# Kernel tuning notes

Measured on AMD Instinct MI355X. Metric: run time of the kernel, lower is better.

Reference implementation:

```python
import jax, jax.numpy as jnp
import numpy as np

NUM_ITERS = 5
NUM_SPATIAL = 3          # S: xyz spatial dims
THETA_ALPHA = 1.0
THETA_BETA = 1.0
THETA_GAMMA = 8.0


def _gauss_filter(f, q):
    """Exact Gaussian filtering (math the permutohedral lattice pl.apply approximates).
    f: [D, N] features, q: [C, N] values.
    out[:, i] = sum_j exp(-0.5 * ||f_i - f_j||^2) * q[:, j]
    """
    f2 = jnp.sum(f * f, axis=0)                       # [N]
    d2 = f2[:, None] + f2[None, :] - 2.0 * (f.T @ f)  # [N, N] squared distances
    K = jnp.exp(-0.5 * d2)                            # symmetric Gaussian kernel
    return q @ K                                      # [C, N]


def setup_inputs() -> dict:
    key = jax.random.key(0)
    k1, k2 = jax.random.split(key)
    C, N, D = 10, 8192, 6
    unaries = jax.random.normal(k1, (C, N), dtype=jnp.float32)
    feat = jax.random.normal(k2, (D, N), dtype=jnp.float32)
    # learned params: diagonal init for filter weights, Potts (-I) compatibility
    spatial_weights = jnp.eye(C, dtype=jnp.float32)
    bilateral_weights = jnp.eye(C, dtype=jnp.float32)
    compatibility_matrix = -jnp.eye(C, dtype=jnp.float32)
    return {
        "unaries": unaries,
        "feat": feat,
        "spatial_weights": spatial_weights,
        "bilateral_weights": bilateral_weights,
        "compatibility_matrix": compatibility_matrix,
    }


def reference(unaries, feat, spatial_weights, bilateral_weights, compatibility_matrix):
    # Pre-scaled features (torch code scales per-iteration, but with
    # theta_alpha=theta_beta=1.0 the in-place aliasing division is a no-op).
    sp_feat = feat[:NUM_SPATIAL] / THETA_GAMMA                      # [S, N]
    bl_feat = jnp.concatenate(
        [feat[:NUM_SPATIAL] / THETA_ALPHA, feat[NUM_SPATIAL:] / THETA_BETA],
        axis=0,
    )                                                               # [S+F, N]

    q = unaries
    for _ in range(NUM_ITERS):
        p = jax.nn.softmax(q, axis=0)                               # over classes
        spatial_out = _gauss_filter(sp_feat, p)                     # [C, N]
        bilateral_out = _gauss_filter(bl_feat, p)                   # [C, N]
        message_passing = spatial_weights @ spatial_out + bilateral_weights @ bilateral_out
        pairwise = compatibility_matrix @ message_passing
        q = unaries - pairwise
    return q
```

## Files before the change

### kernel.cpp

```cpp
#include <hip/hip_runtime.h>
#include <math.h>

#define N 8192
#define C 10
#define NUM_ITERS 5
#define FBLOCK 1024
#define IBLK 32
#define NBLK (N / IBLK)
#define JW (N / 16)
#define NS (JW / 32)
#define LOG2E 1.44269504088896340736f
#define C3 (LOG2E / 64.0f)

typedef _Float16 half8 __attribute__((ext_vector_type(8)));
typedef _Float16 half4 __attribute__((ext_vector_type(4)));
typedef _Float16 half2 __attribute__((ext_vector_type(2)));
typedef float f32x4 __attribute__((ext_vector_type(4)));
typedef float f32x16 __attribute__((ext_vector_type(16)));

#define WS_AJS 0
#define WS_AJB (N * 16)
#define WS_PF0 (N * 32)
#define WS_PF1 (N * 64)
#define PFIDX(n, c) ((((n) >> 4) * 16 + (c)) * 16 + ((n) & 15))

static __device__ __forceinline__ unsigned int pkexp(float a, float b) {
    float ea = __builtin_amdgcn_exp2f(a);
    float eb = __builtin_amdgcn_exp2f(b);
    return __builtin_bit_cast(unsigned int, __builtin_amdgcn_cvt_pkrtz(ea, eb));
}

static __device__ __forceinline__ half8 rdfrag(const unsigned int* R, int q) {
    uint2 lo = *(const uint2*)&R[2 * q];
    uint2 hi = *(const uint2*)&R[8 + 2 * q];
    half2 a = __builtin_bit_cast(half2, lo.x);
    half2 b = __builtin_bit_cast(half2, lo.y);
    half2 c = __builtin_bit_cast(half2, hi.x);
    half2 d = __builtin_bit_cast(half2, hi.y);
    half8 r = {a[0], a[1], b[0], b[1], c[0], c[1], d[0], d[1]};
    return r;
}

__global__ __launch_bounds__(256) void init_kernel(
    const float* __restrict__ unaries, const float* __restrict__ feat,
    half8* __restrict__ ajs8, half8* __restrict__ ajb8,
    _Float16* __restrict__ pf0, _Float16* __restrict__ pf1) {
    int n = blockIdx.x * 256 + threadIdx.x;
    float f6[6];
#pragma unroll
    for (int d = 0; d < 6; ++d) f6[d] = feat[d * N + n];
    float h3 = 0.5f * (f6[0] * f6[0] + f6[1] * f6[1] + f6[2] * f6[2]);
    float h6v = h3 + 0.5f * (f6[3] * f6[3] + f6[4] * f6[4] + f6[5] * f6[5]);
    half8 a = {};
    a[0] = (_Float16)(f6[0] * C3);
    a[1] = (_Float16)(f6[1] * C3);
    a[2] = (_Float16)(f6[2] * C3);
    a[6] = (_Float16)(-h3 * C3);
    a[7] = (_Float16)1.0f;
    ajs8[n] = a;
    half8 b;
#pragma unroll
    for (int d = 0; d < 6; ++d) b[d] = (_Float16)(f6[d] * LOG2E);
    b[6] = (_Float16)(-h6v * LOG2E);
    b[7] = (_Float16)1.0f;
    ajb8[n] = b;

    float q[C];
#pragma unroll
    for (int c = 0; c < C; ++c) q[c] = unaries[c * N + n];
    float m = q[0];
#pragma unroll
    for (int c = 1; c < C; ++c) m = fmaxf(m, q[c]);
    float e[C], s = 0.0f;
#pragma unroll
    for (int c = 0; c < C; ++c) {
        e[c] = __builtin_amdgcn_exp2f((q[c] - m) * LOG2E);
        s += e[c];
    }
    float inv = 1.0f / s;
#pragma unroll
    for (int c = 0; c < C; ++c) pf0[PFIDX(n, c)] = (_Float16)(e[c] * inv);
#pragma unroll
    for (int c = C; c < 16; ++c) {
        pf0[PFIDX(n, c)] = (_Float16)0.0f;
        pf1[PFIDX(n, c)] = (_Float16)0.0f;
    }
}

__global__ __launch_bounds__(FBLOCK, 4) void fused_kernel(
    const float* __restrict__ unaries, const float* __restrict__ feat,
    const float* __restrict__ SW, const float* __restrict__ BW,
    const float* __restrict__ CM,
    const char* __restrict__ ajs_c, const char* __restrict__ ajb_c,
    const _Float16* __restrict__ pf_in, _Float16* __restrict__ pf_out,
    float* __restrict__ out, int is_last) {
    __shared__ union {
        unsigned int wt[16][2][32][18];
        float rbuf[16 * 1024];
    } sm;
    int t = threadIdx.x;
    int i0 = blockIdx.x * IBLK;
    int lane = t & 63;
    int w = t >> 6;
    int il = lane & 15;
    int quad = lane >> 4;
    int li = lane & 31;
    int hs = lane >> 5;
    const f32x4 zero4 = {0.f, 0.f, 0.f, 0.f};
    const f32x16 zero16 = {};

    half8 b1s, b1b;
    {
        int i = i0 + li;
        float g0 = feat[0 * N + i], g1 = feat[1 * N + i], g2 = feat[2 * N + i];
        float g3 = feat[3 * N + i], g4 = feat[4 * N + i], g5 = feat[5 * N + i];
        float h3 = 0.5f * (g0 * g0 + g1 * g1 + g2 * g2);
        float h6v = h3 + 0.5f * (g3 * g3 + g4 * g4 + g5 * g5);
        half4 slo = {(_Float16)g0, (_Float16)g1, (_Float16)g2, (_Float16)0.0f};
        half4 shi = {(_Float16)0.0f, (_Float16)0.0f, (_Float16)1.0f, (_Float16)(-h3 * C3)};
        half4 blo = {(_Float16)g0, (_Float16)g1, (_Float16)g2, (_Float16)g3};
        half4 bhi = {(_Float16)g4, (_Float16)g5, (_Float16)1.0f, (_Float16)(-h6v * LOG2E)};
        half4 sv = hs ? shi : slo;
        half4 bv = hs ? bhi : blo;
        half8 t1 = {sv[0], sv[1], sv[2], sv[3], (_Float16)0.0f, (_Float16)0.0f,
                    (_Float16)0.0f, (_Float16)0.0f};
        half8 t2 = {bv[0], bv[1], bv[2], bv[3], (_Float16)0.0f, (_Float16)0.0f,
                    (_Float16)0.0f, (_Float16)0.0f};
        b1s = t1;
        b1b = t2;
    }

    f32x4 as0 = zero4, as1 = zero4, ab0 = zero4, ab1 = zero4;
    int jw = w * JW;
    const half4* pfv = (const half4*)pf_in;
    unsigned int* Ws = &sm.wt[w][0][li][0];
    unsigned int* Wb = &sm.wt[w][1][li][0];
    const unsigned int* R0s = &sm.wt[w][0][il][0];
    const unsigned int* R1s = &sm.wt[w][0][16 + il][0];
    const unsigned int* R0b = &sm.wt[w][1][il][0];
    const unsigned int* R1b = &sm.wt[w][1][16 + il][0];

    {
        int ph = w & 3;
        if (ph == 1) __builtin_amdgcn_s_sleep(2);
        else if (ph == 2) __builtin_amdgcn_s_sleep(4);
        else if (ph == 3) __builtin_amdgcn_s_sleep(6);
    }

    for (int k = 0; k < NS; ++k) {
        int j0 = jw + k * 32;
        half4 av_s = *(const half4*)(ajs_c + (size_t)(j0 + li) * 16 + hs * 8);
        half4 av_b = *(const half4*)(ajb_c + (size_t)(j0 + li) * 16 + hs * 8);
        half4 cp0 = pfv[((j0 >> 4) * 16 + il) * 4 + quad];
        half4 cp1 = pfv[(((j0 >> 4) + 1) * 16 + il) * 4 + quad];
        half8 A_s = {av_s[0], av_s[1], av_s[2], av_s[3], (_Float16)0.0f,
                     (_Float16)0.0f, (_Float16)0.0f, (_Float16)0.0f};
        half8 A_b = {av_b[0], av_b[1], av_b[2], av_b[3], (_Float16)0.0f,
                     (_Float16)0.0f, (_Float16)0.0f, (_Float16)0.0f};
        half8 Bp = {cp0[0], cp0[1], cp0[2], cp0[3], cp1[0], cp1[1], cp1[2], cp1[3]};

        __builtin_amdgcn_s_setprio(1);
        f32x16 d1s = __builtin_amdgcn_mfma_f32_32x32x16_f16(A_s, b1s, zero16, 0, 0, 0);
        f32x16 d1b = __builtin_amdgcn_mfma_f32_32x32x16_f16(A_b, b1b, zero16, 0, 0, 0);
        __builtin_amdgcn_s_setprio(0);

        {
            uint2 v;
            v.x = pkexp(d1s[0], d1s[1]);  v.y = pkexp(d1s[2], d1s[3]);
            *(uint2*)&Ws[0 + 2 * hs] = v;
            v.x = pkexp(d1s[4], d1s[5]);  v.y = pkexp(d1s[6], d1s[7]);
            *(uint2*)&Ws[4 + 2 * hs] = v;
            v.x = pkexp(d1s[8], d1s[9]);  v.y = pkexp(d1s[10], d1s[11]);
            *(uint2*)&Ws[8 + 2 * hs] = v;
            v.x = pkexp(d1s[12], d1s[13]); v.y = pkexp(d1s[14], d1s[15]);
            *(uint2*)&Ws[12 + 2 * hs] = v;
            v.x = pkexp(d1b[0], d1b[1]);  v.y = pkexp(d1b[2], d1b[3]);
            *(uint2*)&Wb[0 + 2 * hs] = v;
            v.x = pkexp(d1b[4], d1b[5]);  v.y = pkexp(d1b[6], d1b[7]);
            *(uint2*)&Wb[4 + 2 * hs] = v;
            v.x = pkexp(d1b[8], d1b[9]);  v.y = pkexp(d1b[10], d1b[11]);
            *(uint2*)&Wb[8 + 2 * hs] = v;
            v.x = pkexp(d1b[12], d1b[13]); v.y = pkexp(d1b[14], d1b[15]);
            *(uint2*)&Wb[12 + 2 * hs] = v;
        }
        half8 A00 = rdfrag(R0s, quad);
        half8 A01 = rdfrag(R1s, quad);
        half8 A10 = rdfrag(R0b, quad);
        half8 A11 = rdfrag(R1b, quad);
        __builtin_amdgcn_s_setprio(1);
        as0 = __builtin_amdgcn_mfma_f32_16x16x32_f16(A00, Bp, as0, 0, 0, 0);
        as1 = __builtin_amdgcn_mfma_f32_16x16x32_f16(A01, Bp, as1, 0, 0, 0);
        ab0 = __builtin_amdgcn_mfma_f32_16x16x32_f16(A10, Bp, ab0, 0, 0, 0);
        ab1 = __builtin_amdgcn_mfma_f32_16x16x32_f16(A11, Bp, ab1, 0, 0, 0);
        __builtin_amdgcn_s_setprio(0);
    }

    __syncthreads();

    {
        float* rb = sm.rbuf + w * 1024;
#pragma unroll
        for (int r = 0; r < 4; ++r) {
            rb[r * 64 + lane]       = as0[r];
            rb[256 + r * 64 + lane] = as1[r];
            rb[512 + r * 64 + lane] = ab0[r];
            rb[768 + r * 64 + lane] = ab1[r];
        }
    }
    __syncthreads();
    {
        float tot = 0.f;
#pragma unroll
        for (int w2 = 0; w2 < 16; ++w2) tot += sm.rbuf[w2 * 1024 + t];
        sm.rbuf[t] = tot;
    }
    __syncthreads();

    if (t < IBLK) {
        int i = i0 + t;
        int sub = t >> 4, ql = (t & 15) >> 2, rr = t & 3;
        float sp[C], bl[C];
#pragma unroll
        for (int c = 0; c < C; ++c) {
            int base = sub * 256 + rr * 64 + ql * 16 + c;
            sp[c] = sm.rbuf[base];
            bl[c] = sm.rbuf[base + 512];
        }
        float msg[C];
#pragma unroll
        for (int c = 0; c < C; ++c) {
            float m = 0.f;
#pragma unroll
            for (int kk = 0; kk < C; ++kk)
                m += SW[c * C + kk] * sp[kk] + BW[c * C + kk] * bl[kk];
            msg[c] = m;
        }
        float qq[C];
#pragma unroll
        for (int c = 0; c < C; ++c) {
            float pw = 0.f;
#pragma unroll
            for (int kk = 0; kk < C; ++kk) pw += CM[c * C + kk] * msg[kk];
            qq[c] = unaries[c * N + i] - pw;
        }
        if (is_last) {
#pragma unroll
            for (int c = 0; c < C; ++c) out[c * N + i] = qq[c];
        } else {
            float m = qq[0];
#pragma unroll
            for (int c = 1; c < C; ++c) m = fmaxf(m, qq[c]);
            float e[C], s = 0.0f;
#pragma unroll
            for (int c = 0; c < C; ++c) {
                e[c] = __builtin_amdgcn_exp2f((qq[c] - m) * LOG2E);
                s += e[c];
            }
            float inv = 1.0f / s;
#pragma unroll
            for (int c = 0; c < C; ++c) pf_out[PFIDX(i, c)] = (_Float16)(e[c] * inv);
        }
    }
}

extern "C" void kernel_launch(void* const* d_in, const int* in_sizes, int n_in,
                              void* d_out, int out_size, void* d_ws, size_t ws_size,
                              hipStream_t stream) {
    const float* unaries = (const float*)d_in[0];
    const float* feat    = (const float*)d_in[1];
    const float* SW      = (const float*)d_in[2];
    const float* BW      = (const float*)d_in[3];
    const float* CM      = (const float*)d_in[4];
    float* out = (float*)d_out;

    char* ws = (char*)d_ws;
    half8* ajs    = (half8*)(ws + WS_AJS);
    half8* ajb    = (half8*)(ws + WS_AJB);
    _Float16* pf0 = (_Float16*)(ws + WS_PF0);
    _Float16* pf1 = (_Float16*)(ws + WS_PF1);

    init_kernel<<<N / 256, 256, 0, stream>>>(unaries, feat, ajs, ajb, pf0, pf1);
    const _Float16* pin = pf0;
    _Float16* pout = pf1;
    for (int it = 1; it <= NUM_ITERS; ++it) {
        fused_kernel<<<NBLK, FBLOCK, 0, stream>>>(
            unaries, feat, SW, BW, CM, (const char*)ajs, (const char*)ajb,
            pin, pout, out, it == NUM_ITERS ? 1 : 0);
        const _Float16* tmp = pout;
        pout = (_Float16*)pin;
        pin = tmp;
    }
}
```

Baseline: 162.1 us.

## Keep exp weights in registers and use transposed 32x32 MFMA for filtering

Rather than writing the exponentiated kernel weights to shared memory and reading them back as 16x16 MFMA fragments, the second matmul is reformulated so the first MFMA's 32x32 output layout directly serves as the B operand of a 32x32x16 MFMA, with probabilities loaded as the A operand. This removes the per-iteration LDS round trip and the shared weight tile, and shrinks the reduction buffer and its barrier. The cost is larger 32x32 MFMAs that compute padded class rows and a different accumulator layout for the final reduction.

```diff
diff --git a/kernel.cpp b/kernel.cpp
--- a/kernel.cpp
+++ b/kernel.cpp
@@ -17,6 +17,7 @@
 typedef _Float16 half2 __attribute__((ext_vector_type(2)));
 typedef float f32x4 __attribute__((ext_vector_type(4)));
 typedef float f32x16 __attribute__((ext_vector_type(16)));
+typedef unsigned int uint4v __attribute__((ext_vector_type(4)));
 
 #define WS_AJS 0
 #define WS_AJB (N * 16)
@@ -30,15 +31,10 @@
     return __builtin_bit_cast(unsigned int, __builtin_amdgcn_cvt_pkrtz(ea, eb));
 }
 
-static __device__ __forceinline__ half8 rdfrag(const unsigned int* R, int q) {
-    uint2 lo = *(const uint2*)&R[2 * q];
-    uint2 hi = *(const uint2*)&R[8 + 2 * q];
-    half2 a = __builtin_bit_cast(half2, lo.x);
-    half2 b = __builtin_bit_cast(half2, lo.y);
-    half2 c = __builtin_bit_cast(half2, hi.x);
-    half2 d = __builtin_bit_cast(half2, hi.y);
-    half8 r = {a[0], a[1], b[0], b[1], c[0], c[1], d[0], d[1]};
-    return r;
+static __device__ __forceinline__ half8 mk8(unsigned int a, unsigned int b,
+                                            unsigned int c, unsigned int d) {
+    uint4v v = {a, b, c, d};
+    return __builtin_bit_cast(half8, v);
 }
 
 __global__ __launch_bounds__(256) void init_kernel(
@@ -94,19 +90,14 @@
     const char* __restrict__ ajs_c, const char* __restrict__ ajb_c,
     const _Float16* __restrict__ pf_in, _Float16* __restrict__ pf_out,
     float* __restrict__ out, int is_last) {
-    __shared__ union {
-        unsigned int wt[16][2][32][18];
-        float rbuf[16 * 1024];
-    } sm;
+    __shared__ float rbuf[16 * 640];
     int t = threadIdx.x;
     int i0 = blockIdx.x * IBLK;
     int lane = t & 63;
     int w = t >> 6;
-    int il = lane & 15;
-    int quad = lane >> 4;
     int li = lane & 31;
     int hs = lane >> 5;
-    const f32x4 zero4 = {0.f, 0.f, 0.f, 0.f};
+    int cr = li & 15;
     const f32x16 zero16 = {};
 
     half8 b1s, b1b;
@@ -130,15 +121,8 @@
         b1b = t2;
     }
 
-    f32x4 as0 = zero4, as1 = zero4, ab0 = zero4, ab1 = zero4;
+    f32x16 acc_s = zero16, acc_b = zero16;
     int jw = w * JW;
-    const half4* pfv = (const half4*)pf_in;
-    unsigned int* Ws = &sm.wt[w][0][li][0];
-    unsigned int* Wb = &sm.wt[w][1][li][0];
-    const unsigned int* R0s = &sm.wt[w][0][il][0];
-    const unsigned int* R1s = &sm.wt[w][0][16 + il][0];
-    const unsigned int* R0b = &sm.wt[w][1][il][0];
-    const unsigned int* R1b = &sm.wt[w][1][16 + il][0];
 
     {
         int ph = w & 3;
@@ -149,82 +133,80 @@
 
     for (int k = 0; k < NS; ++k) {
         int j0 = jw + k * 32;
+        int jt0 = j0 >> 4;
         half4 av_s = *(const half4*)(ajs_c + (size_t)(j0 + li) * 16 + hs * 8);
         half4 av_b = *(const half4*)(ajb_c + (size_t)(j0 + li) * 16 + hs * 8);
-        half4 cp0 = pfv[((j0 >> 4) * 16 + il) * 4 + quad];
-        half4 cp1 = pfv[(((j0 >> 4) + 1) * 16 + il) * 4 + quad];
+        const _Float16* pr0 = pf_in + (size_t)(jt0 * 16 + cr) * 16;
+        const _Float16* pr1 = pf_in + (size_t)((jt0 + 1) * 16 + cr) * 16;
+        half4 p0l = *(const half4*)&pr0[4 * hs];
+        half4 p0h = *(const half4*)&pr0[8 + 4 * hs];
+        half4 p1l = *(const half4*)&pr1[4 * hs];
+        half4 p1h = *(const half4*)&pr1[8 + 4 * hs];
+        half8 A20 = {p0l[0], p0l[1], p0l[2], p0l[3], p0h[0], p0h[1], p0h[2], p0h[3]};
+        half8 A21 = {p1l[0], p1l[1], p1l[2], p1l[3], p1h[0], p1h[1], p1h[2], p1h[3]};
         half8 A_s = {av_s[0], av_s[1], av_s[2], av_s[3], (_Float16)0.0f,
                      (_Float16)0.0f, (_Float16)0.0f, (_Float16)0.0f};
         half8 A_b = {av_b[0], av_b[1], av_b[2], av_b[3], (_Float16)0.0f,
                      (_Float16)0.0f, (_Float16)0.0f, (_Float16)0.0f};
-        half8 Bp = {cp0[0], cp0[1], cp0[2], cp0[3], cp1[0], cp1[1], cp1[2], cp1[3]};
 
         __builtin_amdgcn_s_setprio(1);
         f32x16 d1s = __builtin_amdgcn_mfma_f32_32x32x16_f16(A_s, b1s, zero16, 0, 0, 0);
         f32x16 d1b = __builtin_amdgcn_mfma_f32_32x32x16_f16(A_b, b1b, zero16, 0, 0, 0);
         __builtin_amdgcn_s_setprio(0);
 
-        {
-            uint2 v;
-            v.x = pkexp(d1s[0], d1s[1]);  v.y = pkexp(d1s[2], d1s[3]);
-            *(uint2*)&Ws[0 + 2 * hs] = v;
-            v.x = pkexp(d1s[4], d1s[5]);  v.y = pkexp(d1s[6], d1s[7]);
-            *(uint2*)&Ws[4 + 2 * hs] = v;
-            v.x = pkexp(d1s[8], d1s[9]);  v.y = pkexp(d1s[10], d1s[11]);
-            *(uint2*)&Ws[8 + 2 * hs] = v;
-            v.x = pkexp(d1s[12], d1s[13]); v.y = pkexp(d1s[14], d1s[15]);
-            *(uint2*)&Ws[12 + 2 * hs] = v;
-            v.x = pkexp(d1b[0], d1b[1]);  v.y = pkexp(d1b[2], d1b[3]);
-            *(uint2*)&Wb[0 + 2 * hs] = v;
-            v.x = pkexp(d1b[4], d1b[5]);  v.y = pkexp(d1b[6], d1b[7]);
-            *(uint2*)&Wb[4 + 2 * hs] = v;
-            v.x = pkexp(d1b[8], d1b[9]);  v.y = pkexp(d1b[10], d1b[11]);
-            *(uint2*)&Wb[8 + 2 * hs] = v;
-            v.x = pkexp(d1b[12], d1b[13]); v.y = pkexp(d1b[14], d1b[15]);
-            *(uint2*)&Wb[12 + 2 * hs] = v;
-        }
-        half8 A00 = rdfrag(R0s, quad);
-        half8 A01 = rdfrag(R1s, quad);
-        half8 A10 = rdfrag(R0b, quad);
-        half8 A11 = rdfrag(R1b, quad);
+        half8 Bs0 = mk8(pkexp(d1s[0], d1s[1]), pkexp(d1s[2], d1s[3]),
+                        pkexp(d1s[4], d1s[5]), pkexp(d1s[6], d1s[7]));
+        half8 Bs1 = mk8(pkexp(d1s[8], d1s[9]), pkexp(d1s[10], d1s[11]),
+                        pkexp(d1s[12], d1s[13]), pkexp(d1s[14], d1s[15]));
+        half8 Bb0 = mk8(pkexp(d1b[0], d1b[1]), pkexp(d1b[2], d1b[3]),
+                        pkexp(d1b[4], d1b[5]), pkexp(d1b[6], d1b[7]));
+        half8 Bb1 = mk8(pkexp(d1b[8], d1b[9]), pkexp(d1b[10], d1b[11]),
+                        pkexp(d1b[12], d1b[13]), pkexp(d1b[14], d1b[15]));
+
         __builtin_amdgcn_s_setprio(1);
-        as0 = __builtin_amdgcn_mfma_f32_16x16x32_f16(A00, Bp, as0, 0, 0, 0);
-        as1 = __builtin_amdgcn_mfma_f32_16x16x32_f16(A01, Bp, as1, 0, 0, 0);
-        ab0 = __builtin_amdgcn_mfma_f32_16x16x32_f16(A10, Bp, ab0, 0, 0, 0);
-        ab1 = __builtin_amdgcn_mfma_f32_16x16x32_f16(A11, Bp, ab1, 0, 0, 0);
+        acc_s = __builtin_amdgcn_mfma_f32_32x32x16_f16(A20, Bs0, acc_s, 0, 0, 0);
+        acc_s = __builtin_amdgcn_mfma_f32_32x32x16_f16(A21, Bs1, acc_s, 0, 0, 0);
+        acc_b = __builtin_amdgcn_mfma_f32_32x32x16_f16(A20, Bb0, acc_b, 0, 0, 0);
+        acc_b = __builtin_amdgcn_mfma_f32_32x32x16_f16(A21, Bb1, acc_b, 0, 0, 0);
         __builtin_amdgcn_s_setprio(0);
     }
 
+    {
+        float* rb = rbuf + w * 640;
+        if (hs == 0) {
+#pragma unroll
+            for (int r = 0; r < 4; ++r) {
+                rb[r * 32 + li]       = acc_s[r];
+                rb[320 + r * 32 + li] = acc_b[r];
+            }
+            rb[8 * 32 + li] = acc_s[4];
+            rb[9 * 32 + li] = acc_s[5];
+            rb[320 + 8 * 32 + li] = acc_b[4];
+            rb[320 + 9 * 32 + li] = acc_b[5];
+        } else {
+#pragma unroll
+            for (int r = 0; r < 4; ++r) {
+                rb[(4 + r) * 32 + li]       = acc_s[r];
+                rb[320 + (4 + r) * 32 + li] = acc_b[r];
+            }
+        }
+    }
     __syncthreads();
-
-    {
-        float* rb = sm.rbuf + w * 1024;
-#pragma unroll
-        for (int r = 0; r < 4; ++r) {
-            rb[r * 64 + lane]       = as0[r];
-            rb[256 + r * 64 + lane] = as1[r];
-            rb[512 + r * 64 + lane] = ab0[r];
-            rb[768 + r * 64 + lane] = ab1[r];
-        }
-    }
-    __syncthreads();
-    {
+    if (t < 640) {
         float tot = 0.f;
 #pragma unroll
-        for (int w2 = 0; w2 < 16; ++w2) tot += sm.rbuf[w2 * 1024 + t];
-        sm.rbuf[t] = tot;
+        for (int w2 = 0; w2 < 16; ++w2) tot += rbuf[w2 * 640 + t];
+        rbuf[t] = tot;
     }
     __syncthreads();
 
     if (t < IBLK) {
         int i = i0 + t;
-        int sub = t >> 4, ql = (t & 15) >> 2, rr = t & 3;
         float sp[C], bl[C];
 #pragma unroll
         for (int c = 0; c < C; ++c) {
-            int base = sub * 256 + rr * 64 + ql * 16 + c;
-            sp[c] = sm.rbuf[base];
-            bl[c] = sm.rbuf[base + 512];
+            sp[c] = rbuf[c * 32 + t];
+            bl[c] = rbuf[320 + c * 32 + t];
         }
         float msg[C];
 #pragma unroll
```

Measured after the change: 161.8 us. No clear change (-0.1%).
